# Optimization experiments

Measured on AMD Instinct MI355X. Metric: run time of the kernel, lower is better.

Reference implementation:

```python
import jax, jax.numpy as jnp
import numpy as np

B, S, D, H = 64, 2048, 512, 512


def setup_inputs() -> dict:
    key = jax.random.key(0)
    ks = jax.random.split(key, 8)
    inp = jax.random.normal(ks[0], (B, D), dtype=jnp.float32)
    context = jax.random.normal(ks[1], (B, S, D), dtype=jnp.float32)
    mask = jax.random.randint(ks[2], (B, S), 0, 2).astype(jnp.int32)
    alpha_mask = jax.random.uniform(ks[3], (B, S), dtype=jnp.float32)
    sd = 1.0 / np.sqrt(D)
    W_in = jax.random.uniform(ks[4], (H, D), minval=-sd, maxval=sd, dtype=jnp.float32)
    b_in = jnp.zeros((H,), dtype=jnp.float32)
    W_ctx = jax.random.uniform(ks[5], (H, D), minval=-sd, maxval=sd, dtype=jnp.float32)  # Conv1d k=1 == pointwise linear
    b_ctx = jnp.zeros((H,), dtype=jnp.float32)
    V = jax.random.uniform(ks[6], (H,), minval=-1.0, maxval=1.0, dtype=jnp.float32)
    return {"input": inp, "context": context, "alpha_mask": alpha_mask,
            "W_in": W_in, "b_in": b_in, "W_ctx": W_ctx, "b_ctx": b_ctx, "V": V,
            "mask": mask}


def reference(input, context, alpha_mask, W_in, b_in, W_ctx, b_ctx, V, mask):
    seq_len = context.shape[1]
    # input_linear: [B, H]
    inp = input @ W_in.T + b_in
    # context_linear (Conv1d kernel=1 over permuted context): [B, H, S]
    ctx = jnp.einsum('hd,bsd->bhs', W_ctx, context) + b_ctx[None, :, None]
    # additive attention energies: V . tanh(inp + ctx) -> [B, S]
    att = jnp.einsum('h,bhs->bs', V, jnp.tanh(inp[:, :, None] + ctx))
    # mask branching (faithful to the torch data-dependent branch, jit-safe):
    # if any(mask) and count(mask) == S: att[mask] = -inf; else: att = att * alpha_mask
    mb = mask != 0
    n_true = jnp.sum(mb)
    take_inf_branch = (n_true > 0) & (n_true == seq_len)
    att = jnp.where(take_inf_branch,
                    jnp.where(mb, -jnp.inf, att),
                    att * alpha_mask)
    alpha = jax.nn.softmax(att, axis=-1)  # [B, S]
    # context vector: bmm(ctx [B,H,S], alpha [B,S,1]) -> [B, H]
    hidden_state = jnp.einsum('bhs,bs->bh', ctx, alpha)
    return hidden_state, alpha
```

## Files before the change

kernel.cpp:

```cpp
#include <hip/hip_runtime.h>
#include <math.h>

#define B 64
#define S 2048
#define D 512
#define H 512

#define WSC 128
#define LDA 40

typedef _Float16 f16x8 __attribute__((ext_vector_type(8)));
typedef __fp16 fp16x2 __attribute__((ext_vector_type(2)));
typedef float f32x4 __attribute__((ext_vector_type(4)));

#define WS_PART_OFF (512 * 1024)
#define WS_CNT_OFF  (512 * 1024 + 4 * 1024 * 1024)

#define GLOAD16(g, l)                                                          \
    __builtin_amdgcn_global_load_lds(                                          \
        (const __attribute__((address_space(1))) uint32_t*)(g),                \
        (__attribute__((address_space(3))) uint32_t*)(l), 16, 0, 0)

__global__ __launch_bounds__(256) void k_prep(
        const float* __restrict__ Wc, _Float16* __restrict__ wsB,
        const float* __restrict__ input, const float* __restrict__ W_in,
        const float* __restrict__ b_in, float* __restrict__ out_inp,
        const int* __restrict__ mask, int* __restrict__ cntArr) {
    const int bid = blockIdx.x;
    const int tid = threadIdx.x;

    if (bid < 128) {
        const int slot = bid * 256 + tid;
        const int st   = slot >> 11;
        const int rem  = slot & 2047;
        const int hg   = rem >> 6;
        const int lane = rem & 63;
        const int h  = hg * 16 + (lane & 15);
        const int k0 = st * 32 + (lane >> 4) * 8;
        const float* src = Wc + (size_t)h * D + k0;
        float4 f0 = *(const float4*)src;
        float4 f1 = *(const float4*)(src + 4);
        f16x8 v;
        v[0] = (_Float16)f0.x; v[1] = (_Float16)f0.y;
        v[2] = (_Float16)f0.z; v[3] = (_Float16)f0.w;
        v[4] = (_Float16)f1.x; v[5] = (_Float16)f1.y;
        v[6] = (_Float16)f1.z; v[7] = (_Float16)f1.w;
        *(f16x8*)(wsB + (size_t)slot * 8) = v;
    } else if (bid < 192) {
        const int b = bid - 128;
        __shared__ float xrow[D];
        for (int d = tid; d < D; d += 256) xrow[d] = input[(size_t)b * D + d];
        __syncthreads();
        for (int h = tid; h < H; h += 256) {
            const float* w = W_in + (size_t)h * D;
            float acc = 0.f;
            #pragma unroll 4
            for (int d = 0; d < D; d += 4) {
                float4 wv = *(const float4*)(w + d);
                acc += wv.x * xrow[d] + wv.y * xrow[d + 1] + wv.z * xrow[d + 2] + wv.w * xrow[d + 3];
            }
            out_inp[(size_t)b * H + h] = acc + b_in[h];
        }
    } else {
        const int i0 = (bid - 192) * 2048;
        int local = 0;
        #pragma unroll
        for (int it = 0; it < 8; ++it)
            local += (mask[i0 + it * 256 + tid] != 0) ? 1 : 0;
        #pragma unroll
        for (int off = 32; off; off >>= 1) local += __shfl_down(local, off, 64);
        __shared__ int ired[4];
        if ((tid & 63) == 0) ired[tid >> 6] = local;
        __syncthreads();
        if (tid == 0) cntArr[bid - 192] = ired[0] + ired[1] + ired[2] + ired[3];
    }
}

__global__ __launch_bounds__(256) void k_energy(
        const float* __restrict__ ctx,
        const _Float16* __restrict__ WcP,
        const float* __restrict__ bc,
        const float* __restrict__ inp,
        const float* __restrict__ V,
        float* __restrict__ att) {
    __shared__ alignas(16) _Float16 Alds[2][64 * LDA];
    __shared__ alignas(16) _Float16 Blds[2][8192];
    __shared__ float red[4][64];

    const int tid = threadIdx.x;
    const int hb    = blockIdx.x & 1;
    const int stile = blockIdx.x >> 1;
    const int b  = stile >> 5;
    const int s0 = (stile & 31) << 6;

    const int arow = tid >> 2;
    const int akq  = tid & 3;
    const int lane = tid & 63;
    const int w    = tid >> 6;
    const int lrow = lane & 15;
    const int kblk = lane >> 4;

    f32x4 acc[4][4] = {};

    const float* ctx_src = ctx + ((size_t)b * S + s0 + arow) * D + akq * 8;
    const _Float16* Bg = WcP + ((size_t)(hb * 16 + w * 4) * 64 + lane) * 8;

    #pragma unroll
    for (int i = 0; i < 4; ++i)
        GLOAD16(Bg + (size_t)(i * 64) * 8, &Blds[0][(w * 4 + i) * 512]);
    {
        float4 f0 = *(const float4*)ctx_src;
        float4 f1 = *(const float4*)(ctx_src + 4);
        union { fp16x2 h2[4]; f16x8 v; } u;
        u.h2[0] = __builtin_amdgcn_cvt_pkrtz(f0.x, f0.y);
        u.h2[1] = __builtin_amdgcn_cvt_pkrtz(f0.z, f0.w);
        u.h2[2] = __builtin_amdgcn_cvt_pkrtz(f1.x, f1.y);
        u.h2[3] = __builtin_amdgcn_cvt_pkrtz(f1.z, f1.w);
        *(f16x8*)&Alds[0][arow * LDA + akq * 8] = u.v;
    }
    __syncthreads();

    #pragma unroll 1
    for (int kt = 0; kt < 16; ++kt) {
        const int cur = kt & 1;

        float4 nf0, nf1;
        if (kt < 15) {
            #pragma unroll
            for (int i = 0; i < 4; ++i)
                GLOAD16(Bg + ((size_t)(kt + 1) * 2048 + i * 64) * 8,
                        &Blds[cur ^ 1][(w * 4 + i) * 512]);
            nf0 = *(const float4*)(ctx_src + (kt + 1) * 32);
            nf1 = *(const float4*)(ctx_src + (kt + 1) * 32 + 4);
        }

        f16x8 bfr[4];
        #pragma unroll
        for (int n = 0; n < 4; ++n)
            bfr[n] = *(const f16x8*)&Blds[cur][(w * 4 + n) * 512 + lane * 8];
        f16x8 afr[4];
        #pragma unroll
        for (int m = 0; m < 4; ++m)
            afr[m] = *(const f16x8*)&Alds[cur][(m * 16 + lrow) * LDA + kblk * 8];

        #pragma unroll
        for (int m = 0; m < 4; ++m)
            #pragma unroll
            for (int n = 0; n < 4; ++n)
                acc[m][n] = __builtin_amdgcn_mfma_f32_16x16x32_f16(
                    afr[m], bfr[n], acc[m][n], 0, 0, 0);

        if (kt < 15) {
            union { fp16x2 h2[4]; f16x8 v; } u;
            u.h2[0] = __builtin_amdgcn_cvt_pkrtz(nf0.x, nf0.y);
            u.h2[1] = __builtin_amdgcn_cvt_pkrtz(nf0.z, nf0.w);
            u.h2[2] = __builtin_amdgcn_cvt_pkrtz(nf1.x, nf1.y);
            u.h2[3] = __builtin_amdgcn_cvt_pkrtz(nf1.z, nf1.w);
            *(f16x8*)&Alds[cur ^ 1][arow * LDA + akq * 8] = u.v;
        }
        __syncthreads();
    }

    float ps_[4][4] = {};
    #pragma unroll
    for (int n = 0; n < 4; ++n) {
        const int h = hb * 256 + (w * 4 + n) * 16 + lrow;
        const float ib = inp[(size_t)b * H + h] + bc[h];
        const float v = V[h];
        #pragma unroll
        for (int m = 0; m < 4; ++m)
            #pragma unroll
            for (int r = 0; r < 4; ++r) {
                const float x = acc[m][n][r] + ib;
                const float t = 1.f - 2.f / (1.f + __expf(2.f * x));
                ps_[m][r] += v * t;
            }
    }
    #pragma unroll
    for (int off = 1; off < 16; off <<= 1)
        #pragma unroll
        for (int m = 0; m < 4; ++m)
            #pragma unroll
            for (int r = 0; r < 4; ++r)
                ps_[m][r] += __shfl_xor(ps_[m][r], off, 64);
    if (lrow == 0) {
        #pragma unroll
        for (int m = 0; m < 4; ++m)
            #pragma unroll
            for (int r = 0; r < 4; ++r)
                red[w][m * 16 + kblk * 4 + r] = ps_[m][r];
    }
    __syncthreads();
    if (tid < 64) {
        const float sum = red[0][tid] + red[1][tid] + red[2][tid] + red[3][tid];
        atomicAdd(att + (size_t)b * S + s0 + tid, sum);
    }
}

__global__ __launch_bounds__(256) void k_softmax(
        const int* __restrict__ mask,
        const float* __restrict__ amask,
        const int* __restrict__ cntArr,
        float* __restrict__ att) {
    const int b = blockIdx.x;
    const int tid = threadIdx.x;
    __shared__ float sh[S];
    __shared__ float fredm[4];
    __shared__ float freds[4];

    int n_true = 0;
    #pragma unroll
    for (int i = 0; i < 64; ++i) n_true += cntArr[i];
    const bool inf_branch = (n_true > 0) && (n_true == S);

    const float NEG_INF = -__builtin_inff();
    for (int s = tid; s < S; s += 256) {
        const float raw = att[(size_t)b * S + s];
        float v;
        if (inf_branch)
            v = mask[(size_t)b * S + s] ? NEG_INF : raw;
        else
            v = raw * amask[(size_t)b * S + s];
        sh[s] = v;
    }
    __syncthreads();

    float mx = NEG_INF;
    for (int s = tid; s < S; s += 256) mx = fmaxf(mx, sh[s]);
    #pragma unroll
    for (int off = 32; off; off >>= 1) mx = fmaxf(mx, __shfl_down(mx, off, 64));
    if ((tid & 63) == 0) fredm[tid >> 6] = mx;
    __syncthreads();
    mx = fmaxf(fmaxf(fredm[0], fredm[1]), fmaxf(fredm[2], fredm[3]));

    float lsum = 0.f;
    for (int s = tid; s < S; s += 256) {
        const float e = expf(sh[s] - mx);
        sh[s] = e;
        lsum += e;
    }
    #pragma unroll
    for (int off = 32; off; off >>= 1) lsum += __shfl_down(lsum, off, 64);
    if ((tid & 63) == 0) freds[tid >> 6] = lsum;
    __syncthreads();
    const float total = freds[0] + freds[1] + freds[2] + freds[3];
    const float rinv = 1.f / total;

    for (int s = tid; s < S; s += 256)
        att[(size_t)b * S + s] = sh[s] * rinv;
}

__global__ __launch_bounds__(256) void k_wsum(
        const float* __restrict__ ctx,
        const float* __restrict__ alpha,
        float* __restrict__ part) {
    const int chunk = blockIdx.x & 15;
    const int b = blockIdx.x >> 4;
    const int s0 = chunk * WSC;
    const int tid = threadIdx.x;
    __shared__ float al[WSC];
    if (tid < WSC) al[tid] = alpha[(size_t)b * S + s0 + tid];
    __syncthreads();

    const int half = tid >> 7;
    const int dq = (tid & 127) * 4;
    const float* base = ctx + ((size_t)b * S + s0 + half) * D + dq;
    float4 acc = {0.f, 0.f, 0.f, 0.f};
    #pragma unroll 4
    for (int i = 0; i < WSC / 2; ++i) {
        float4 v = *(const float4*)(base + (size_t)i * 2 * D);
        const float a = al[i * 2 + half];
        acc.x += a * v.x; acc.y += a * v.y; acc.z += a * v.z; acc.w += a * v.w;
    }
    __shared__ float cb[2][D];
    *(float4*)&cb[half][dq] = acc;
    __syncthreads();
    if (tid < 128) {
        const int d = tid * 4;
        float4 p0 = *(const float4*)&cb[0][d];
        float4 p1 = *(const float4*)&cb[1][d];
        float4 o = {p0.x + p1.x, p0.y + p1.y, p0.z + p1.z, p0.w + p1.w};
        *(float4*)(part + ((size_t)chunk * B + b) * D + d) = o;
    }
}

__global__ __launch_bounds__(256) void k_out(
        const float* __restrict__ part,
        const float* __restrict__ Wc,
        const float* __restrict__ bc,
        float* __restrict__ hidden) {
    const int b = blockIdx.x;
    const int tid = threadIdx.x;
    __shared__ float cb[D];
    for (int d = tid; d < D; d += 256) {
        float s = 0.f;
        #pragma unroll
        for (int c = 0; c < 16; ++c)
            s += part[((size_t)c * B + b) * D + d];
        cb[d] = s;
    }
    __syncthreads();
    for (int h = tid; h < H; h += 256) {
        const float* w = Wc + (size_t)h * D;
        float acc = 0.f;
        #pragma unroll 4
        for (int d = 0; d < D; d += 4) {
            float4 wv = *(const float4*)(w + d);
            acc += wv.x * cb[d] + wv.y * cb[d + 1] + wv.z * cb[d + 2] + wv.w * cb[d + 3];
        }
        hidden[(size_t)b * H + h] = acc + bc[h];
    }
}

extern "C" void kernel_launch(void* const* d_in, const int* in_sizes, int n_in,
                              void* d_out, int out_size, void* d_ws, size_t ws_size,
                              hipStream_t stream) {
    const float* input = (const float*)d_in[0];
    const float* ctx   = (const float*)d_in[1];
    const float* amask = (const float*)d_in[2];
    const float* W_in  = (const float*)d_in[3];
    const float* b_in  = (const float*)d_in[4];
    const float* W_ctx = (const float*)d_in[5];
    const float* b_ctx = (const float*)d_in[6];
    const float* V     = (const float*)d_in[7];
    const int*   mask  = (const int*)d_in[8];

    float* out = (float*)d_out;
    float* hidden = out;
    float* alpha  = out + B * H;

    _Float16* wsB    = (_Float16*)d_ws;
    float*    part   = (float*)((char*)d_ws + WS_PART_OFF);
    int*      cntArr = (int*)((char*)d_ws + WS_CNT_OFF);

    k_prep<<<dim3(256), dim3(256), 0, stream>>>(
        W_ctx, wsB, input, W_in, b_in, hidden, mask, cntArr);

    (void)hipMemsetAsync(alpha, 0, (size_t)B * S * sizeof(float), stream);
    k_energy<<<dim3(B * S / 64 * 2), dim3(256), 0, stream>>>(
        ctx, wsB, b_ctx, hidden, V, alpha);

    k_softmax<<<dim3(B), dim3(256), 0, stream>>>(mask, amask, cntArr, alpha);

    k_wsum<<<dim3(16 * B), dim3(256), 0, stream>>>(ctx, alpha, part);

    k_out<<<dim3(B), dim3(256), 0, stream>>>(part, W_ctx, b_ctx, hidden);
}
```

Measured before the change: 251.9 us.

## Cover all H per block in energy kernel, stage fp32 ctx via async LDS loads

The energy kernel now uses 512-thread blocks that compute all 512 hidden units for a 64-row S tile. Each block reads context once instead of twice, which removes the atomicAdd accumulation and the memset of the attention buffer. Context tiles are copied as fp32 straight into XOR-swizzled LDS with global_load_lds in 128-wide K chunks, double-buffered, and converted to fp16 when fragments are read. W fragments are loaded directly from global/L2 instead of LDS, which adds global load latency inside the MFMA loop, and the 64KB of LDS per block may limit occupancy.

```diff
diff --git a/kernel.cpp b/kernel.cpp
--- a/kernel.cpp
+++ b/kernel.cpp
@@ -7,7 +7,6 @@
 #define H 512
 
 #define WSC 128
-#define LDA 40
 
 typedef _Float16 f16x8 __attribute__((ext_vector_type(8)));
 typedef __fp16 fp16x2 __attribute__((ext_vector_type(2)));
@@ -76,95 +75,88 @@
     }
 }
 
-__global__ __launch_bounds__(256) void k_energy(
+__global__ __launch_bounds__(512, 4) void k_energy(
         const float* __restrict__ ctx,
         const _Float16* __restrict__ WcP,
         const float* __restrict__ bc,
         const float* __restrict__ inp,
         const float* __restrict__ V,
         float* __restrict__ att) {
-    __shared__ alignas(16) _Float16 Alds[2][64 * LDA];
-    __shared__ alignas(16) _Float16 Blds[2][8192];
-    __shared__ float red[4][64];
-
-    const int tid = threadIdx.x;
-    const int hb    = blockIdx.x & 1;
-    const int stile = blockIdx.x >> 1;
-    const int b  = stile >> 5;
-    const int s0 = (stile & 31) << 6;
-
-    const int arow = tid >> 2;
-    const int akq  = tid & 3;
+    __shared__ alignas(16) float Af[2][64 * 128];
+    __shared__ float red[8][64];
+
+    const int tid = threadIdx.x;
+    const int b  = blockIdx.x >> 5;
+    const int s0 = (blockIdx.x & 31) << 6;
+
     const int lane = tid & 63;
     const int w    = tid >> 6;
     const int lrow = lane & 15;
     const int kblk = lane >> 4;
+    const int sw   = (lrow & 7) << 2;
 
     f32x4 acc[4][4] = {};
 
-    const float* ctx_src = ctx + ((size_t)b * S + s0 + arow) * D + akq * 8;
-    const _Float16* Bg = WcP + ((size_t)(hb * 16 + w * 4) * 64 + lane) * 8;
-
-    #pragma unroll
-    for (int i = 0; i < 4; ++i)
-        GLOAD16(Bg + (size_t)(i * 64) * 8, &Blds[0][(w * 4 + i) * 512]);
-    {
-        float4 f0 = *(const float4*)ctx_src;
-        float4 f1 = *(const float4*)(ctx_src + 4);
-        union { fp16x2 h2[4]; f16x8 v; } u;
-        u.h2[0] = __builtin_amdgcn_cvt_pkrtz(f0.x, f0.y);
-        u.h2[1] = __builtin_amdgcn_cvt_pkrtz(f0.z, f0.w);
-        u.h2[2] = __builtin_amdgcn_cvt_pkrtz(f1.x, f1.y);
-        u.h2[3] = __builtin_amdgcn_cvt_pkrtz(f1.z, f1.w);
-        *(f16x8*)&Alds[0][arow * LDA + akq * 8] = u.v;
-    }
+    const _Float16* Bbase = WcP + ((size_t)(w * 4) * 64 + lane) * 8;
+
+    #define STAGE_CHUNK(BUF, CK)                                               \
+        _Pragma("unroll")                                                      \
+        for (int gi = 0; gi < 4; ++gi) {                                       \
+            const int row_ = w * 8 + gi * 2 + (lane >> 5);                     \
+            const int g_ = (lane & 31) ^ ((row_ & 7) << 2);                    \
+            GLOAD16(ctx + ((size_t)b * S + s0 + row_) * D + (CK) * 128 + g_ * 4, \
+                    &Af[BUF][(w * 8 + gi * 2) * 128]);                         \
+        }
+
+    STAGE_CHUNK(0, 0)
     __syncthreads();
 
     #pragma unroll 1
-    for (int kt = 0; kt < 16; ++kt) {
-        const int cur = kt & 1;
-
-        float4 nf0, nf1;
-        if (kt < 15) {
-            #pragma unroll
-            for (int i = 0; i < 4; ++i)
-                GLOAD16(Bg + ((size_t)(kt + 1) * 2048 + i * 64) * 8,
-                        &Blds[cur ^ 1][(w * 4 + i) * 512]);
-            nf0 = *(const float4*)(ctx_src + (kt + 1) * 32);
-            nf1 = *(const float4*)(ctx_src + (kt + 1) * 32 + 4);
+    for (int c = 0; c < 4; ++c) {
+        const int cur = c & 1;
+
+        if (c < 3) STAGE_CHUNK(cur ^ 1, c + 1)
+
+        #pragma unroll
+        for (int st = 0; st < 4; ++st) {
+            const int stg = c * 4 + st;
+            f16x8 bfr[4];
+            #pragma unroll
+            for (int n = 0; n < 4; ++n)
+                bfr[n] = *(const f16x8*)(Bbase + ((size_t)stg * 2048 + n * 64) * 8);
+
+            f16x8 afr[4];
+            #pragma unroll
+            for (int m = 0; m < 4; ++m) {
+                const int ph0 = (st * 8 + kblk * 2) ^ sw;
+                const int ph1 = (st * 8 + kblk * 2 + 1) ^ sw;
+                const float* rb = &Af[cur][(m * 16 + lrow) * 128];
+                float4 f0 = *(const float4*)(rb + ph0 * 4);
+                float4 f1 = *(const float4*)(rb + ph1 * 4);
+                union { fp16x2 h2[4]; f16x8 v; } u;
+                u.h2[0] = __builtin_amdgcn_cvt_pkrtz(f0.x, f0.y);
+                u.h2[1] = __builtin_amdgcn_cvt_pkrtz(f0.z, f0.w);
+                u.h2[2] = __builtin_amdgcn_cvt_pkrtz(f1.x, f1.y);
+                u.h2[3] = __builtin_amdgcn_cvt_pkrtz(f1.z, f1.w);
+                afr[m] = u.v;
+            }
+
+            #pragma unroll
+            for (int m = 0; m < 4; ++m)
+                #pragma unroll
+                for (int n = 0; n < 4; ++n)
+                    acc[m][n] = __builtin_amdgcn_mfma_f32_16x16x32_f16(
+                        afr[m], bfr[n], acc[m][n], 0, 0, 0);
         }
 
-        f16x8 bfr[4];
-        #pragma unroll
-        for (int n = 0; n < 4; ++n)
-            bfr[n] = *(const f16x8*)&Blds[cur][(w * 4 + n) * 512 + lane * 8];
-        f16x8 afr[4];
-        #pragma unroll
-        for (int m = 0; m < 4; ++m)
-            afr[m] = *(const f16x8*)&Alds[cur][(m * 16 + lrow) * LDA + kblk * 8];
-
-        #pragma unroll
-        for (int m = 0; m < 4; ++m)
-            #pragma unroll
-            for (int n = 0; n < 4; ++n)
-                acc[m][n] = __builtin_amdgcn_mfma_f32_16x16x32_f16(
-                    afr[m], bfr[n], acc[m][n], 0, 0, 0);
-
-        if (kt < 15) {
-            union { fp16x2 h2[4]; f16x8 v; } u;
-            u.h2[0] = __builtin_amdgcn_cvt_pkrtz(nf0.x, nf0.y);
-            u.h2[1] = __builtin_amdgcn_cvt_pkrtz(nf0.z, nf0.w);
-            u.h2[2] = __builtin_amdgcn_cvt_pkrtz(nf1.x, nf1.y);
-            u.h2[3] = __builtin_amdgcn_cvt_pkrtz(nf1.z, nf1.w);
-            *(f16x8*)&Alds[cur ^ 1][arow * LDA + akq * 8] = u.v;
-        }
         __syncthreads();
     }
+    #undef STAGE_CHUNK
 
     float ps_[4][4] = {};
     #pragma unroll
     for (int n = 0; n < 4; ++n) {
-        const int h = hb * 256 + (w * 4 + n) * 16 + lrow;
+        const int h = w * 64 + n * 16 + lrow;
         const float ib = inp[(size_t)b * H + h] + bc[h];
         const float v = V[h];
         #pragma unroll
@@ -192,8 +184,10 @@
     }
     __syncthreads();
     if (tid < 64) {
-        const float sum = red[0][tid] + red[1][tid] + red[2][tid] + red[3][tid];
-        atomicAdd(att + (size_t)b * S + s0 + tid, sum);
+        float sum = 0.f;
+        #pragma unroll
+        for (int i = 0; i < 8; ++i) sum += red[i][tid];
+        att[(size_t)b * S + s0 + tid] = sum;
     }
 }
 
@@ -336,8 +330,7 @@
     k_prep<<<dim3(256), dim3(256), 0, stream>>>(
         W_ctx, wsB, input, W_in, b_in, hidden, mask, cntArr);
 
-    (void)hipMemsetAsync(alpha, 0, (size_t)B * S * sizeof(float), stream);
-    k_energy<<<dim3(B * S / 64 * 2), dim3(256), 0, stream>>>(
+    k_energy<<<dim3(B * S / 64), dim3(512), 0, stream>>>(
         ctx, wsB, b_ctx, hidden, V, alpha);
 
     k_softmax<<<dim3(B), dim3(256), 0, stream>>>(mask, amask, cntArr, alpha);
```

New measurement: 248.7 us. Within noise of the previous version (-1.3%).
